# Kernel optimization log

Measured on AMD Instinct MI355X. Metric: run time of the kernel, lower is better.

The kernel has to match this reference:

```python
import jax, jax.numpy as jnp
import numpy as np

# config constants (match init_kwargs)
D_MODEL = 1024        # hidden_size
D_FF = 2048           # intermediate_size
N_EXPERTS = 8         # num_local_experts
TOP_K = 2             # num_experts_per_tok


def setup_inputs() -> dict:
    key = jax.random.key(0)
    k1, k2, k3, k4 = jax.random.split(key, 4)
    layer_input = jax.random.normal(k1, (2, 2048, D_MODEL), dtype=jnp.float32)
    # router: nn.Linear(hidden_size, num_experts, bias=False) -> weight [E, D]
    router_weight = jax.random.normal(k2, (N_EXPERTS, D_MODEL), dtype=jnp.float32) * 0.02
    # ParallelExperts weights: [num_experts, out_features, in_features]
    w_in = jax.random.normal(k3, (N_EXPERTS, 2 * D_FF, D_MODEL), dtype=jnp.float32) * 0.02
    w_out = jax.random.normal(k4, (N_EXPERTS, D_MODEL, D_FF), dtype=jnp.float32) * 0.02
    return {"layer_input": layer_input, "router_weight": router_weight,
            "w_in": w_in, "w_out": w_out}


def _moe_forward(x, router_weight, w_in, w_out):
    # x: [T, D]
    T = x.shape[0]
    logits = x @ router_weight.T                       # [T, E] router logits
    top_vals, top_idx = jax.lax.top_k(logits, TOP_K)   # [T, K]
    gates_k = jax.nn.softmax(top_vals, axis=-1).astype(x.dtype)
    # dense gate matrix: zero for unselected experts -> identical math to
    # the gather / grouped-GEMM / scatter-add path in the torch module.
    gates = jnp.zeros((T, N_EXPERTS), x.dtype).at[
        jnp.arange(T)[:, None], top_idx].set(gates_k)  # [T, E]
    # grouped GEMM #1: [E, T, 2*D_FF]
    h = jnp.einsum('td,efd->etf', x, w_in)
    h1, h2 = jnp.split(h, 2, axis=-1)
    act = jax.nn.silu(h1) * h2                         # SwiGLU: silu(a)*b
    # grouped GEMM #2: [E, T, D]
    y = jnp.einsum('eth,edh->etd', act, w_out)
    # gate-weighted combine (scatter-add equivalent)
    out = jnp.einsum('etd,te->td', y, gates)           # [T, D]
    return out, logits


def reference(layer_input, router_weight, w_in, w_out):
    bsz, length, emb = layer_input.shape
    x = layer_input.reshape(-1, emb)
    out, router_logits = _moe_forward(x, router_weight, w_in, w_out)
    return out.reshape(bsz, length, emb), router_logits
```

## Files before the change

### kernel.cpp

```cpp
#include <hip/hip_runtime.h>
#include <stdint.h>

#define N_TOK   4096
#define DMODEL  1024
#define DFF     2048
#define N_EXP   8
#define N_SLOTS (N_TOK * 2)
#define ROWS_PAD (N_SLOTS + 128)

typedef __bf16 bf16x8 __attribute__((ext_vector_type(8)));
typedef float  f32x4  __attribute__((ext_vector_type(4)));
typedef unsigned short u16;
typedef unsigned short u16x8 __attribute__((ext_vector_type(8)));
typedef unsigned short u16x4 __attribute__((ext_vector_type(4)));

__device__ __forceinline__ u16 f2bf(float f) {
    union { float f; uint32_t u; } v; v.f = f;
    uint32_t r = v.u + 0x7FFFu + ((v.u >> 16) & 1u);
    return (u16)(r >> 16);
}
__device__ __forceinline__ float bf2f(u16 u) {
    union { uint32_t u; float f; } v; v.u = ((uint32_t)u) << 16;
    return v.f;
}

__device__ __forceinline__ void g2l16(const void* gp, void* lp) {
    auto g = reinterpret_cast<const __attribute__((address_space(1))) unsigned int*>(
        reinterpret_cast<uintptr_t>(gp));
    auto l = reinterpret_cast<__attribute__((address_space(3))) unsigned int*>(
        reinterpret_cast<uintptr_t>(lp));
    __builtin_amdgcn_global_load_lds(g, l, 16, 0, 0);
}

__device__ __forceinline__ int idx64(int r, int cb) {
    return r * 64 + ((cb ^ (r & 7)) * 8);
}

#define WIN_V8  (N_EXP * 2 * DFF * DMODEL / 8)
#define WOUT_V8 (N_EXP * DMODEL * DFF / 8)
#define CVT_BLOCKS ((WIN_V8 + WOUT_V8) / 256)
#define RTR_BLOCKS (N_TOK / 4)

__global__ void cvt_router_kernel(const float4* __restrict__ win, const float4* __restrict__ wout,
                                  u16x8* __restrict__ winbf, u16x8* __restrict__ woutbf,
                                  const float* __restrict__ x, const float* __restrict__ rw,
                                  float* __restrict__ logits, int* __restrict__ tok_expert,
                                  float* __restrict__ tok_gate) {
    int bid = blockIdx.x;
    if (bid < CVT_BLOCKS) {
        int i = bid * 256 + threadIdx.x;
        const float4* s; u16x8* d; int k;
        if (i < WIN_V8) { s = win;  d = winbf;  k = i; }
        else            { s = wout; d = woutbf; k = i - WIN_V8; }
        float4 a = s[k * 2];
        float4 b = s[k * 2 + 1];
        u16x8 o = { f2bf(a.x), f2bf(a.y), f2bf(a.z), f2bf(a.w),
                    f2bf(b.x), f2bf(b.y), f2bf(b.z), f2bf(b.w) };
        d[k] = o;
        return;
    }
    int t = (bid - CVT_BLOCKS) * 4 + (threadIdx.x >> 6);
    int lane = threadIdx.x & 63;
    const float* xr = x + (size_t)t * DMODEL;
    float acc[N_EXP];
#pragma unroll
    for (int e = 0; e < N_EXP; ++e) acc[e] = 0.f;
    for (int i = 0; i < DMODEL / 64; ++i) {
        int k = lane + i * 64;
        float xv = xr[k];
#pragma unroll
        for (int e = 0; e < N_EXP; ++e) acc[e] += xv * rw[e * DMODEL + k];
    }
#pragma unroll
    for (int e = 0; e < N_EXP; ++e) {
        float v = acc[e];
        for (int off = 32; off > 0; off >>= 1) v += __shfl_down(v, off, 64);
        acc[e] = v;
    }
    if (lane == 0) {
        float* lg = logits + (size_t)t * N_EXP;
#pragma unroll
        for (int e = 0; e < N_EXP; ++e) lg[e] = acc[e];
        int e0 = 0; float v0 = acc[0];
#pragma unroll
        for (int e = 1; e < N_EXP; ++e) if (acc[e] > v0) { v0 = acc[e]; e0 = e; }
        int e1 = -1; float v1 = -3.0e38f;
#pragma unroll
        for (int e = 0; e < N_EXP; ++e) if (e != e0 && acc[e] > v1) { v1 = acc[e]; e1 = e; }
        float ex = expf(v1 - v0);
        tok_expert[t * 2 + 0] = e0;  tok_gate[t * 2 + 0] = 1.0f / (1.0f + ex);
        tok_expert[t * 2 + 1] = e1;  tok_gate[t * 2 + 1] = ex / (1.0f + ex);
    }
}

__global__ void scan_kernel(const int* __restrict__ tok_expert, int* __restrict__ offs,
                            int* __restrict__ inv) {
    __shared__ int cnt[N_EXP][257];
    __shared__ int soffs[N_EXP];
    int tid = threadIdx.x;
    int base = tid * 32;
    int loc[N_EXP];
#pragma unroll
    for (int e = 0; e < N_EXP; ++e) loc[e] = 0;
    for (int i = 0; i < 32; ++i) {
        int ex = tok_expert[base + i];
#pragma unroll
        for (int e = 0; e < N_EXP; ++e) loc[e] += (ex == e);
    }
#pragma unroll
    for (int e = 0; e < N_EXP; ++e) cnt[e][tid] = loc[e];
    __syncthreads();
    if (tid < N_EXP) {
        int running = 0;
        for (int t = 0; t < 256; ++t) { int c = cnt[tid][t]; cnt[tid][t] = running; running += c; }
        cnt[tid][256] = running;
    }
    __syncthreads();
    if (tid == 0) {
        int s = 0;
        for (int e = 0; e < N_EXP; ++e) { offs[e] = s; soffs[e] = s; s += cnt[e][256]; }
        offs[N_EXP] = s;
    }
    __syncthreads();
#pragma unroll
    for (int e = 0; e < N_EXP; ++e) loc[e] = 0;
    for (int i = 0; i < 32; ++i) {
        int ex = tok_expert[base + i];
        int row = 0;
#pragma unroll
        for (int e = 0; e < N_EXP; ++e)
            if (ex == e) { row = soffs[e] + cnt[e][tid] + loc[e]; loc[e]++; }
        inv[base + i] = row;
    }
}

__global__ void gather_kernel(const float* __restrict__ x, const int* __restrict__ inv,
                              u16* __restrict__ Abf) {
    int t = blockIdx.x;
    int r0 = inv[t * 2];
    int r1 = inv[t * 2 + 1];
    float4 v = ((const float4*)(x + (size_t)t * DMODEL))[threadIdx.x];
    u16x4 o = { f2bf(v.x), f2bf(v.y), f2bf(v.z), f2bf(v.w) };
    *(u16x4*)(Abf + (size_t)r0 * DMODEL + threadIdx.x * 4) = o;
    *(u16x4*)(Abf + (size_t)r1 * DMODEL + threadIdx.x * 4) = o;
}

__global__ __launch_bounds__(256, 4)
void gemm1_kernel(const u16* __restrict__ Abf, const u16* __restrict__ winbf,
                  u16* __restrict__ act, const int* __restrict__ offs) {
    int bid = blockIdx.x;
    int nt = bid & 31;
    int mg = (bid >> 5) & 7;
    int e  = bid >> 8;
    int cnt = offs[e + 1] - offs[e];
    int n0 = nt * 64;
    const u16* wb = winbf + (size_t)e * (2 * DFF) * DMODEL;

    __shared__ u16 lsA[128 * 64];
    __shared__ u16 lsB[2][64 * 64];

    int tid = threadIdx.x, lane = tid & 63, wave = tid >> 6;
    int wm = wave >> 1, wn = wave & 1;
    int s_r8 = lane >> 3;
    int s_cb = ((lane & 7) ^ (lane >> 3)) * 8;

    for (int mt = mg; mt * 128 < cnt; mt += 8) {
        int row0 = offs[e] + mt * 128;
        f32x4 acc[2][4][2];
        f32x4 zero = {0.f, 0.f, 0.f, 0.f};
#pragma unroll
        for (int h = 0; h < 2; ++h)
#pragma unroll
            for (int mi = 0; mi < 4; ++mi)
#pragma unroll
                for (int ni = 0; ni < 2; ++ni) acc[h][mi][ni] = zero;

        for (int kk = 0; kk < DMODEL / 64; ++kk) {
            int k0 = kk * 64;
#pragma unroll
            for (int q = 0; q < 4; ++q) {
                int R0 = wave * 32 + q * 8;
                g2l16(Abf + (size_t)(row0 + R0 + s_r8) * DMODEL + k0 + s_cb, &lsA[R0 * 64]);
            }
#pragma unroll
            for (int h = 0; h < 2; ++h)
#pragma unroll
                for (int q = 0; q < 2; ++q) {
                    int R0 = wave * 16 + q * 8;
                    g2l16(wb + (size_t)(h * DFF + n0 + R0 + s_r8) * DMODEL + k0 + s_cb,
                          &lsB[h][R0 * 64]);
                }
            __syncthreads();
#pragma unroll
            for (int kh = 0; kh < 2; ++kh) {
                int cb = kh * 4 + (lane >> 4);
                bf16x8 afr[4];
#pragma unroll
                for (int mi = 0; mi < 4; ++mi)
                    afr[mi] = *(const bf16x8*)&lsA[idx64(wm * 64 + mi * 16 + (lane & 15), cb)];
#pragma unroll
                for (int h = 0; h < 2; ++h)
#pragma unroll
                    for (int ni = 0; ni < 2; ++ni) {
                        bf16x8 bfr = *(const bf16x8*)&lsB[h][idx64(wn * 32 + ni * 16 + (lane & 15), cb)];
#pragma unroll
                        for (int mi = 0; mi < 4; ++mi)
                            acc[h][mi][ni] = __builtin_amdgcn_mfma_f32_16x16x32_bf16(
                                afr[mi], bfr, acc[h][mi][ni], 0, 0, 0);
                    }
            }
            __syncthreads();
        }
        int mmax = cnt - mt * 128;
#pragma unroll
        for (int mi = 0; mi < 4; ++mi)
#pragma unroll
            for (int i = 0; i < 4; ++i) {
                int rl = wm * 64 + mi * 16 + (lane >> 4) * 4 + i;
                if (rl < mmax) {
                    size_t rp = (size_t)(row0 + rl) * DFF;
#pragma unroll
                    for (int ni = 0; ni < 2; ++ni) {
                        int col = n0 + wn * 32 + ni * 16 + (lane & 15);
                        float a = acc[0][mi][ni][i];
                        float b = acc[1][mi][ni][i];
                        float sv = a / (1.0f + __expf(-a));
                        act[rp + col] = f2bf(sv * b);
                    }
                }
            }
    }
}

__global__ __launch_bounds__(256, 4)
void gemm2_kernel(const u16* __restrict__ act, const u16* __restrict__ woutbf,
                  u16* __restrict__ ybA, u16* __restrict__ ybB,
                  const int* __restrict__ offs) {
    int bid = blockIdx.x;
    int nt = bid & 7;
    int mg = (bid >> 3) & 7;
    int kc = (bid >> 6) & 1;
    int e  = bid >> 7;
    int cnt = offs[e + 1] - offs[e];
    int n0 = nt * 128;
    const u16* wb = woutbf + (size_t)e * DMODEL * DFF;

    __shared__ u16 lsA[128 * 64];
    __shared__ u16 lsB[128 * 64];

    int tid = threadIdx.x, lane = tid & 63, wave = tid >> 6;
    int wm = wave >> 1, wn = wave & 1;
    int s_r8 = lane >> 3;
    int s_cb = ((lane & 7) ^ (lane >> 3)) * 8;
    u16* yb = kc ? ybB : ybA;

    for (int mt = mg; mt * 128 < cnt; mt += 8) {
        int row0 = offs[e] + mt * 128;
        f32x4 acc[4][4];
        f32x4 zero = {0.f, 0.f, 0.f, 0.f};
#pragma unroll
        for (int mi = 0; mi < 4; ++mi)
#pragma unroll
            for (int ni = 0; ni < 4; ++ni) acc[mi][ni] = zero;

        for (int kk = kc * 16; kk < kc * 16 + 16; ++kk) {
            int k0 = kk * 64;
#pragma unroll
            for (int q = 0; q < 4; ++q) {
                int R0 = wave * 32 + q * 8;
                g2l16(act + (size_t)(row0 + R0 + s_r8) * DFF + k0 + s_cb, &lsA[R0 * 64]);
                g2l16(wb + (size_t)(n0 + R0 + s_r8) * DFF + k0 + s_cb, &lsB[R0 * 64]);
            }
            __syncthreads();
#pragma unroll
            for (int kh = 0; kh < 2; ++kh) {
                int cb = kh * 4 + (lane >> 4);
                bf16x8 afr[4];
#pragma unroll
                for (int mi = 0; mi < 4; ++mi)
                    afr[mi] = *(const bf16x8*)&lsA[idx64(wm * 64 + mi * 16 + (lane & 15), cb)];
#pragma unroll
                for (int ni = 0; ni < 4; ++ni) {
                    bf16x8 bfr = *(const bf16x8*)&lsB[idx64(wn * 64 + ni * 16 + (lane & 15), cb)];
#pragma unroll
                    for (int mi = 0; mi < 4; ++mi)
                        acc[mi][ni] = __builtin_amdgcn_mfma_f32_16x16x32_bf16(
                            afr[mi], bfr, acc[mi][ni], 0, 0, 0);
                }
            }
            __syncthreads();
        }
        int mmax = cnt - mt * 128;
#pragma unroll
        for (int mi = 0; mi < 4; ++mi)
#pragma unroll
            for (int i = 0; i < 4; ++i) {
                int rl = wm * 64 + mi * 16 + (lane >> 4) * 4 + i;
                if (rl < mmax) {
                    u16* yrow = yb + (size_t)(row0 + rl) * DMODEL;
#pragma unroll
                    for (int ni = 0; ni < 4; ++ni) {
                        int col = n0 + wn * 64 + ni * 16 + (lane & 15);
                        yrow[col] = f2bf(acc[mi][ni][i]);
                    }
                }
            }
    }
}

__global__ void combine_kernel(const u16* __restrict__ ybA, const u16* __restrict__ ybB,
                               const int* __restrict__ inv, const float* __restrict__ tok_gate,
                               float* __restrict__ out) {
    int t = blockIdx.x;
    int tid = threadIdx.x;
    __shared__ int sr0, sr1;
    __shared__ float sg0, sg1;
    if (tid == 0) {
        sr0 = inv[t * 2];  sr1 = inv[t * 2 + 1];
        sg0 = tok_gate[t * 2];  sg1 = tok_gate[t * 2 + 1];
    }
    __syncthreads();
    int d = tid * 4;
    u16x4 a0 = *(const u16x4*)(ybA + (size_t)sr0 * DMODEL + d);
    u16x4 b0 = *(const u16x4*)(ybB + (size_t)sr0 * DMODEL + d);
    u16x4 a1 = *(const u16x4*)(ybA + (size_t)sr1 * DMODEL + d);
    u16x4 b1 = *(const u16x4*)(ybB + (size_t)sr1 * DMODEL + d);
    float4 o;
    o.x = sg0 * (bf2f(a0.x) + bf2f(b0.x)) + sg1 * (bf2f(a1.x) + bf2f(b1.x));
    o.y = sg0 * (bf2f(a0.y) + bf2f(b0.y)) + sg1 * (bf2f(a1.y) + bf2f(b1.y));
    o.z = sg0 * (bf2f(a0.z) + bf2f(b0.z)) + sg1 * (bf2f(a1.z) + bf2f(b1.z));
    o.w = sg0 * (bf2f(a0.w) + bf2f(b0.w)) + sg1 * (bf2f(a1.w) + bf2f(b1.w));
    *(float4*)(out + (size_t)t * DMODEL + d) = o;
}

extern "C" void kernel_launch(void* const* d_in, const int* in_sizes, int n_in,
                              void* d_out, int out_size, void* d_ws, size_t ws_size,
                              hipStream_t stream) {
    const float* x    = (const float*)d_in[0];
    const float* rw   = (const float*)d_in[1];
    const float* win  = (const float*)d_in[2];
    const float* wout = (const float*)d_in[3];
    float* out    = (float*)d_out;
    float* logits = out + (size_t)N_TOK * DMODEL;

    char* ws = (char*)d_ws;
    size_t o = 0;
    auto alloc = [&](size_t bytes) -> void* {
        void* p = ws + o;
        o = (o + bytes + 255) & ~(size_t)255;
        return p;
    };
    u16*   Abf      = (u16*)  alloc((size_t)ROWS_PAD * DMODEL * 2);
    u16*   actbuf   = (u16*)  alloc((size_t)ROWS_PAD * DFF * 2);
    u16*   winbf    = (u16*)  alloc((size_t)N_EXP * 2 * DFF * DMODEL * 2);
    u16*   woutbf   = (u16*)  alloc((size_t)N_EXP * DMODEL * DFF * 2);
    int*   offs     = (int*)  alloc(16 * 4);
    int*   inv      = (int*)  alloc(N_SLOTS * 4);
    int*   tok_exp  = (int*)  alloc(N_SLOTS * 4);
    float* tok_gate = (float*)alloc(N_SLOTS * 4);
    u16*   ybA      = winbf;
    u16*   ybB      = winbf + (size_t)ROWS_PAD * DMODEL;
    (void)ws_size; (void)in_sizes; (void)n_in; (void)out_size;

    cvt_router_kernel<<<CVT_BLOCKS + RTR_BLOCKS, 256, 0, stream>>>(
        (const float4*)win, (const float4*)wout, (u16x8*)winbf, (u16x8*)woutbf,
        x, rw, logits, tok_exp, tok_gate);
    scan_kernel<<<1, 256, 0, stream>>>(tok_exp, offs, inv);
    gather_kernel<<<N_TOK, 256, 0, stream>>>(x, inv, Abf);
    gemm1_kernel<<<8 * 8 * 32, 256, 0, stream>>>(Abf, winbf, actbuf, offs);
    gemm2_kernel<<<8 * 2 * 8 * 8, 256, 0, stream>>>(actbuf, woutbf, ybA, ybB, offs);
    combine_kernel<<<N_TOK, 256, 0, stream>>>(ybA, ybB, inv, tok_gate, out);
}
```

Measured before the change: 460.0 us.

## Schedule grouped GEMMs over a flat per-tile table instead of per-expert loops

The scan kernel now builds a compact table of (expert, start row, valid rows) for every 128-row M tile across all experts. Both grouped GEMM kernels launch one block per (tile, N-tile[, K-half]) and index into this table, replacing the per-expert grid with a strided M-tile loop. This is meant to balance load when expert token counts are skewed, since one heavily loaded expert no longer serialises its tiles inside a few blocks. The cost is a serial tile-table build in a single thread and some early-exiting blocks, and MAX_TILES=72 must cover the worst-case tile count.

```diff
diff --git a/kernel.cpp b/kernel.cpp
--- a/kernel.cpp
+++ b/kernel.cpp
@@ -7,6 +7,7 @@
 #define N_EXP   8
 #define N_SLOTS (N_TOK * 2)
 #define ROWS_PAD (N_SLOTS + 128)
+#define MAX_TILES 72
 
 typedef __bf16 bf16x8 __attribute__((ext_vector_type(8)));
 typedef float  f32x4  __attribute__((ext_vector_type(4)));
@@ -94,7 +95,7 @@
 }
 
 __global__ void scan_kernel(const int* __restrict__ tok_expert, int* __restrict__ offs,
-                            int* __restrict__ inv) {
+                            int* __restrict__ inv, int* __restrict__ tiletab) {
     __shared__ int cnt[N_EXP][257];
     __shared__ int soffs[N_EXP];
     int tid = threadIdx.x;
@@ -120,6 +121,19 @@
         int s = 0;
         for (int e = 0; e < N_EXP; ++e) { offs[e] = s; soffs[e] = s; s += cnt[e][256]; }
         offs[N_EXP] = s;
+        int n = 0;
+        for (int e = 0; e < N_EXP; ++e) {
+            int c = cnt[e][256];
+            int r0 = soffs[e];
+            for (int m = 0; m * 128 < c; ++m) {
+                int rem = c - m * 128;
+                tiletab[4 + n * 4 + 0] = e;
+                tiletab[4 + n * 4 + 1] = r0 + m * 128;
+                tiletab[4 + n * 4 + 2] = rem < 128 ? rem : 128;
+                ++n;
+            }
+        }
+        tiletab[0] = n;
     }
     __syncthreads();
 #pragma unroll
@@ -147,12 +161,14 @@
 
 __global__ __launch_bounds__(256, 4)
 void gemm1_kernel(const u16* __restrict__ Abf, const u16* __restrict__ winbf,
-                  u16* __restrict__ act, const int* __restrict__ offs) {
+                  u16* __restrict__ act, const int* __restrict__ tiletab) {
     int bid = blockIdx.x;
     int nt = bid & 31;
-    int mg = (bid >> 5) & 7;
-    int e  = bid >> 8;
-    int cnt = offs[e + 1] - offs[e];
+    int ti = bid >> 5;
+    if (ti >= tiletab[0]) return;
+    int e    = tiletab[4 + ti * 4 + 0];
+    int row0 = tiletab[4 + ti * 4 + 1];
+    int mmax = tiletab[4 + ti * 4 + 2];
     int n0 = nt * 64;
     const u16* wb = winbf + (size_t)e * (2 * DFF) * DMODEL;
 
@@ -164,84 +180,82 @@
     int s_r8 = lane >> 3;
     int s_cb = ((lane & 7) ^ (lane >> 3)) * 8;
 
-    for (int mt = mg; mt * 128 < cnt; mt += 8) {
-        int row0 = offs[e] + mt * 128;
-        f32x4 acc[2][4][2];
-        f32x4 zero = {0.f, 0.f, 0.f, 0.f};
+    f32x4 acc[2][4][2];
+    f32x4 zero = {0.f, 0.f, 0.f, 0.f};
+#pragma unroll
+    for (int h = 0; h < 2; ++h)
+#pragma unroll
+        for (int mi = 0; mi < 4; ++mi)
+#pragma unroll
+            for (int ni = 0; ni < 2; ++ni) acc[h][mi][ni] = zero;
+
+    for (int kk = 0; kk < DMODEL / 64; ++kk) {
+        int k0 = kk * 64;
+#pragma unroll
+        for (int q = 0; q < 4; ++q) {
+            int R0 = wave * 32 + q * 8;
+            g2l16(Abf + (size_t)(row0 + R0 + s_r8) * DMODEL + k0 + s_cb, &lsA[R0 * 64]);
+        }
 #pragma unroll
         for (int h = 0; h < 2; ++h)
 #pragma unroll
+            for (int q = 0; q < 2; ++q) {
+                int R0 = wave * 16 + q * 8;
+                g2l16(wb + (size_t)(h * DFF + n0 + R0 + s_r8) * DMODEL + k0 + s_cb,
+                      &lsB[h][R0 * 64]);
+            }
+        __syncthreads();
+#pragma unroll
+        for (int kh = 0; kh < 2; ++kh) {
+            int cb = kh * 4 + (lane >> 4);
+            bf16x8 afr[4];
+#pragma unroll
             for (int mi = 0; mi < 4; ++mi)
-#pragma unroll
-                for (int ni = 0; ni < 2; ++ni) acc[h][mi][ni] = zero;
-
-        for (int kk = 0; kk < DMODEL / 64; ++kk) {
-            int k0 = kk * 64;
-#pragma unroll
-            for (int q = 0; q < 4; ++q) {
-                int R0 = wave * 32 + q * 8;
-                g2l16(Abf + (size_t)(row0 + R0 + s_r8) * DMODEL + k0 + s_cb, &lsA[R0 * 64]);
-            }
+                afr[mi] = *(const bf16x8*)&lsA[idx64(wm * 64 + mi * 16 + (lane & 15), cb)];
 #pragma unroll
             for (int h = 0; h < 2; ++h)
 #pragma unroll
-                for (int q = 0; q < 2; ++q) {
-                    int R0 = wave * 16 + q * 8;
-                    g2l16(wb + (size_t)(h * DFF + n0 + R0 + s_r8) * DMODEL + k0 + s_cb,
-                          &lsB[h][R0 * 64]);
+                for (int ni = 0; ni < 2; ++ni) {
+                    bf16x8 bfr = *(const bf16x8*)&lsB[h][idx64(wn * 32 + ni * 16 + (lane & 15), cb)];
+#pragma unroll
+                    for (int mi = 0; mi < 4; ++mi)
+                        acc[h][mi][ni] = __builtin_amdgcn_mfma_f32_16x16x32_bf16(
+                            afr[mi], bfr, acc[h][mi][ni], 0, 0, 0);
                 }
-            __syncthreads();
-#pragma unroll
-            for (int kh = 0; kh < 2; ++kh) {
-                int cb = kh * 4 + (lane >> 4);
-                bf16x8 afr[4];
-#pragma unroll
-                for (int mi = 0; mi < 4; ++mi)
-                    afr[mi] = *(const bf16x8*)&lsA[idx64(wm * 64 + mi * 16 + (lane & 15), cb)];
-#pragma unroll
-                for (int h = 0; h < 2; ++h)
-#pragma unroll
-                    for (int ni = 0; ni < 2; ++ni) {
-                        bf16x8 bfr = *(const bf16x8*)&lsB[h][idx64(wn * 32 + ni * 16 + (lane & 15), cb)];
-#pragma unroll
-                        for (int mi = 0; mi < 4; ++mi)
-                            acc[h][mi][ni] = __builtin_amdgcn_mfma_f32_16x16x32_bf16(
-                                afr[mi], bfr, acc[h][mi][ni], 0, 0, 0);
-                    }
-            }
-            __syncthreads();
-        }
-        int mmax = cnt - mt * 128;
-#pragma unroll
-        for (int mi = 0; mi < 4; ++mi)
-#pragma unroll
-            for (int i = 0; i < 4; ++i) {
-                int rl = wm * 64 + mi * 16 + (lane >> 4) * 4 + i;
-                if (rl < mmax) {
-                    size_t rp = (size_t)(row0 + rl) * DFF;
-#pragma unroll
-                    for (int ni = 0; ni < 2; ++ni) {
-                        int col = n0 + wn * 32 + ni * 16 + (lane & 15);
-                        float a = acc[0][mi][ni][i];
-                        float b = acc[1][mi][ni][i];
-                        float sv = a / (1.0f + __expf(-a));
-                        act[rp + col] = f2bf(sv * b);
-                    }
+        }
+        __syncthreads();
+    }
+#pragma unroll
+    for (int mi = 0; mi < 4; ++mi)
+#pragma unroll
+        for (int i = 0; i < 4; ++i) {
+            int rl = wm * 64 + mi * 16 + (lane >> 4) * 4 + i;
+            if (rl < mmax) {
+                size_t rp = (size_t)(row0 + rl) * DFF;
+#pragma unroll
+                for (int ni = 0; ni < 2; ++ni) {
+                    int col = n0 + wn * 32 + ni * 16 + (lane & 15);
+                    float a = acc[0][mi][ni][i];
+                    float b = acc[1][mi][ni][i];
+                    float sv = a / (1.0f + __expf(-a));
+                    act[rp + col] = f2bf(sv * b);
                 }
             }
-    }
+        }
 }
 
 __global__ __launch_bounds__(256, 4)
 void gemm2_kernel(const u16* __restrict__ act, const u16* __restrict__ woutbf,
                   u16* __restrict__ ybA, u16* __restrict__ ybB,
-                  const int* __restrict__ offs) {
+                  const int* __restrict__ tiletab) {
     int bid = blockIdx.x;
-    int nt = bid & 7;
-    int mg = (bid >> 3) & 7;
-    int kc = (bid >> 6) & 1;
-    int e  = bid >> 7;
-    int cnt = offs[e + 1] - offs[e];
+    int kc = bid & 1;
+    int nt = (bid >> 1) & 7;
+    int ti = bid >> 4;
+    if (ti >= tiletab[0]) return;
+    int e    = tiletab[4 + ti * 4 + 0];
+    int row0 = tiletab[4 + ti * 4 + 1];
+    int mmax = tiletab[4 + ti * 4 + 2];
     int n0 = nt * 128;
     const u16* wb = woutbf + (size_t)e * DMODEL * DFF;
 
@@ -254,58 +268,54 @@
     int s_cb = ((lane & 7) ^ (lane >> 3)) * 8;
     u16* yb = kc ? ybB : ybA;
 
-    for (int mt = mg; mt * 128 < cnt; mt += 8) {
-        int row0 = offs[e] + mt * 128;
-        f32x4 acc[4][4];
-        f32x4 zero = {0.f, 0.f, 0.f, 0.f};
-#pragma unroll
-        for (int mi = 0; mi < 4; ++mi)
-#pragma unroll
-            for (int ni = 0; ni < 4; ++ni) acc[mi][ni] = zero;
-
-        for (int kk = kc * 16; kk < kc * 16 + 16; ++kk) {
-            int k0 = kk * 64;
-#pragma unroll
-            for (int q = 0; q < 4; ++q) {
-                int R0 = wave * 32 + q * 8;
-                g2l16(act + (size_t)(row0 + R0 + s_r8) * DFF + k0 + s_cb, &lsA[R0 * 64]);
-                g2l16(wb + (size_t)(n0 + R0 + s_r8) * DFF + k0 + s_cb, &lsB[R0 * 64]);
-            }
-            __syncthreads();
-#pragma unroll
-            for (int kh = 0; kh < 2; ++kh) {
-                int cb = kh * 4 + (lane >> 4);
-                bf16x8 afr[4];
+    f32x4 acc[4][4];
+    f32x4 zero = {0.f, 0.f, 0.f, 0.f};
+#pragma unroll
+    for (int mi = 0; mi < 4; ++mi)
+#pragma unroll
+        for (int ni = 0; ni < 4; ++ni) acc[mi][ni] = zero;
+
+    for (int kk = kc * 16; kk < kc * 16 + 16; ++kk) {
+        int k0 = kk * 64;
+#pragma unroll
+        for (int q = 0; q < 4; ++q) {
+            int R0 = wave * 32 + q * 8;
+            g2l16(act + (size_t)(row0 + R0 + s_r8) * DFF + k0 + s_cb, &lsA[R0 * 64]);
+            g2l16(wb + (size_t)(n0 + R0 + s_r8) * DFF + k0 + s_cb, &lsB[R0 * 64]);
+        }
+        __syncthreads();
+#pragma unroll
+        for (int kh = 0; kh < 2; ++kh) {
+            int cb = kh * 4 + (lane >> 4);
+            bf16x8 afr[4];
+#pragma unroll
+            for (int mi = 0; mi < 4; ++mi)
+                afr[mi] = *(const bf16x8*)&lsA[idx64(wm * 64 + mi * 16 + (lane & 15), cb)];
+#pragma unroll
+            for (int ni = 0; ni < 4; ++ni) {
+                bf16x8 bfr = *(const bf16x8*)&lsB[idx64(wn * 64 + ni * 16 + (lane & 15), cb)];
 #pragma unroll
                 for (int mi = 0; mi < 4; ++mi)
-                    afr[mi] = *(const bf16x8*)&lsA[idx64(wm * 64 + mi * 16 + (lane & 15), cb)];
+                    acc[mi][ni] = __builtin_amdgcn_mfma_f32_16x16x32_bf16(
+                        afr[mi], bfr, acc[mi][ni], 0, 0, 0);
+            }
+        }
+        __syncthreads();
+    }
+#pragma unroll
+    for (int mi = 0; mi < 4; ++mi)
+#pragma unroll
+        for (int i = 0; i < 4; ++i) {
+            int rl = wm * 64 + mi * 16 + (lane >> 4) * 4 + i;
+            if (rl < mmax) {
+                u16* yrow = yb + (size_t)(row0 + rl) * DMODEL;
 #pragma unroll
                 for (int ni = 0; ni < 4; ++ni) {
-                    bf16x8 bfr = *(const bf16x8*)&lsB[idx64(wn * 64 + ni * 16 + (lane & 15), cb)];
-#pragma unroll
-                    for (int mi = 0; mi < 4; ++mi)
-                        acc[mi][ni] = __builtin_amdgcn_mfma_f32_16x16x32_bf16(
-                            afr[mi], bfr, acc[mi][ni], 0, 0, 0);
+                    int col = n0 + wn * 64 + ni * 16 + (lane & 15);
+                    yrow[col] = f2bf(acc[mi][ni][i]);
                 }
             }
-            __syncthreads();
-        }
-        int mmax = cnt - mt * 128;
-#pragma unroll
-        for (int mi = 0; mi < 4; ++mi)
-#pragma unroll
-            for (int i = 0; i < 4; ++i) {
-                int rl = wm * 64 + mi * 16 + (lane >> 4) * 4 + i;
-                if (rl < mmax) {
-                    u16* yrow = yb + (size_t)(row0 + rl) * DMODEL;
-#pragma unroll
-                    for (int ni = 0; ni < 4; ++ni) {
-                        int col = n0 + wn * 64 + ni * 16 + (lane & 15);
-                        yrow[col] = f2bf(acc[mi][ni][i]);
-                    }
-                }
-            }
-    }
+        }
 }
 
 __global__ void combine_kernel(const u16* __restrict__ ybA, const u16* __restrict__ ybB,
@@ -358,6 +368,7 @@
     int*   inv      = (int*)  alloc(N_SLOTS * 4);
     int*   tok_exp  = (int*)  alloc(N_SLOTS * 4);
     float* tok_gate = (float*)alloc(N_SLOTS * 4);
+    int*   tiletab  = (int*)  alloc((4 + MAX_TILES * 4) * 4);
     u16*   ybA      = winbf;
     u16*   ybB      = winbf + (size_t)ROWS_PAD * DMODEL;
     (void)ws_size; (void)in_sizes; (void)n_in; (void)out_size;
@@ -365,9 +376,9 @@
     cvt_router_kernel<<<CVT_BLOCKS + RTR_BLOCKS, 256, 0, stream>>>(
         (const float4*)win, (const float4*)wout, (u16x8*)winbf, (u16x8*)woutbf,
         x, rw, logits, tok_exp, tok_gate);
-    scan_kernel<<<1, 256, 0, stream>>>(tok_exp, offs, inv);
+    scan_kernel<<<1, 256, 0, stream>>>(tok_exp, offs, inv, tiletab);
     gather_kernel<<<N_TOK, 256, 0, stream>>>(x, inv, Abf);
-    gemm1_kernel<<<8 * 8 * 32, 256, 0, stream>>>(Abf, winbf, actbuf, offs);
-    gemm2_kernel<<<8 * 2 * 8 * 8, 256, 0, stream>>>(actbuf, woutbf, ybA, ybB, offs);
+    gemm1_kernel<<<MAX_TILES * 32, 256, 0, stream>>>(Abf, winbf, actbuf, tiletab);
+    gemm2_kernel<<<MAX_TILES * 16, 256, 0, stream>>>(actbuf, woutbf, ybA, ybB, tiletab);
     combine_kernel<<<N_TOK, 256, 0, stream>>>(ybA, ybB, inv, tok_gate, out);
 }
```

Result: faster. 430.3 us (-6.5%).
